# Kernel tuning notes

Measured on AMD Instinct MI355X. Metric: run time of the kernel, lower is better.

## Reference

```python
import jax, jax.numpy as jnp
import numpy as np

B, T, IN, H, OUT = 256, 512, 9, 512, 3


def setup_inputs() -> dict:
    key = jax.random.key(0)
    ks = jax.random.split(key, 7)
    s = 0.05  # keep gates in a sane range
    return {
        "x": jax.random.normal(ks[0], (B, T, IN), dtype=jnp.float32),
        "W_ih": jax.random.normal(ks[1], (4 * H, IN), dtype=jnp.float32) * s,
        "W_hh": jax.random.normal(ks[2], (4 * H, H), dtype=jnp.float32) * s,
        "b_ih": jax.random.normal(ks[3], (4 * H,), dtype=jnp.float32) * s,
        "b_hh": jax.random.normal(ks[4], (4 * H,), dtype=jnp.float32) * s,
        "W_fc": jax.random.normal(ks[5], (OUT, H), dtype=jnp.float32) * s,
        "b_fc": jax.random.normal(ks[6], (OUT,), dtype=jnp.float32) * s,
        "horizon": 10,
    }


def reference(x, W_ih, W_hh, b_ih, b_hh, W_fc, b_fc, horizon):
    Bn, Tn, _ = x.shape
    Hn = W_hh.shape[1]
    On = W_fc.shape[0]
    # branch condition depends only on the static step index -> precompute mask
    idx = np.arange(Tn)
    use_raw = jnp.asarray((idx < 5) | (idx % int(horizon) == 0))  # [T]

    def step(carry, inp):
        hx, cx, prev_out = carry
        x_t, raw = inp  # x_t: [B, IN], raw: scalar bool
        # else-branch input: previous fc output (3) ++ last 6 state features -> 9
        alt = jnp.concatenate([prev_out, x_t[:, On:]], axis=1)
        xin = jnp.where(raw, x_t, alt)
        gates = xin @ W_ih.T + b_ih + hx @ W_hh.T + b_hh  # [B, 4H]
        i, f, g, o = jnp.split(gates, 4, axis=1)
        cx2 = jax.nn.sigmoid(f) * cx + jax.nn.sigmoid(i) * jnp.tanh(g)
        hx2 = jax.nn.sigmoid(o) * jnp.tanh(cx2)
        out = hx2 @ W_fc.T + b_fc  # [B, OUT]
        return (hx2, cx2, out), out

    init = (
        jnp.zeros((Bn, Hn), x.dtype),
        jnp.zeros((Bn, Hn), x.dtype),
        jnp.zeros((Bn, On), x.dtype),
    )
    x_tb = jnp.swapaxes(x, 0, 1)  # [T, B, IN]
    _, outs = jax.lax.scan(step, init, (x_tb, use_raw))
    return jnp.swapaxes(outs, 0, 1)  # [B, T, OUT]
```

## Files before the change

kernel.cpp:

```cpp
#include <hip/hip_runtime.h>

typedef __attribute__((ext_vector_type(8))) short bf16x8;
typedef __attribute__((ext_vector_type(4))) float f32x4;

#define NTT 512
#define NH  512
#define NIN 9
#define NO  3
#define MEMBERS 32
#define MROWS   32
#define HPW     16

__device__ __forceinline__ short f2bf(float f) {
  unsigned u = __builtin_bit_cast(unsigned, f);
  u = (u + 0x7fffu + ((u >> 16) & 1u)) >> 16;
  return (short)u;
}
__device__ __forceinline__ float bf2f(short s) {
  unsigned u = ((unsigned)(unsigned short)s) << 16;
  return __builtin_bit_cast(float, u);
}
__device__ __forceinline__ float sigf(float x) { return 1.f / (1.f + __expf(-x)); }
__device__ __forceinline__ float tanh_fast(float x) { return 1.f - 2.f / (1.f + __expf(2.f * x)); }

__global__ __launch_bounds__(256, 1) void lstm_tagged(
    const float* __restrict__ x, const float* __restrict__ W_ih,
    const float* __restrict__ W_hh, const float* __restrict__ b_ih,
    const float* __restrict__ b_hh, const float* __restrict__ W_fc,
    const float* __restrict__ b_fc, const int* __restrict__ horizon,
    float* __restrict__ out, unsigned* __restrict__ ws32) {
  const int tid  = threadIdx.x;
  const int bid  = blockIdx.x;
  const int g    = bid >> 5;
  const int w    = bid & 31;
  const int wid  = tid >> 6;
  const int lane = tid & 63;
  const int l15  = lane & 15;
  const int quad = lane >> 4;
  const int hl   = tid & 15;
  const int b0   = tid >> 4;
  const int hg   = w * HPW + hl;

  unsigned* tbuf0 = ws32;
  unsigned* tbuf1 = ws32 + 131072;

  __shared__ __align__(16) unsigned short hbuf[32][520];
  __shared__ __align__(16) float gbuf[4][16][36];
  __shared__ float fcbuf[4][32][4];
  __shared__ float xbuf[32][NIN];
  __shared__ float xw[64][NIN];
  __shared__ float bsl[64];

  bf16x8 Bhi[16], Blo[16];
#pragma unroll
  for (int kt = 0; kt < 16; ++kt) {
    bf16x8 vh, vl;
    const int row = wid * NH + w * HPW + l15;
#pragma unroll
    for (int j = 0; j < 8; ++j) {
      int k = kt * 32 + quad * 8 + j;
      float v = W_hh[(size_t)row * NH + k];
      short hi = f2bf(v);
      vh[j] = hi; vl[j] = f2bf(v - bf2f(hi));
    }
    Bhi[kt] = vh; Blo[kt] = vl;
  }
  bf16x8 Fhi[4], Flo[4];
#pragma unroll
  for (int kk = 0; kk < 4; ++kk) {
    bf16x8 vh, vl;
#pragma unroll
    for (int j = 0; j < 8; ++j) {
      int k = (wid * 4 + kk) * 32 + quad * 8 + j;
      float v = (l15 < NO) ? W_fc[(size_t)l15 * NH + k] : 0.f;
      short hi = f2bf(v);
      vh[j] = hi; vl[j] = f2bf(v - bf2f(hi));
    }
    Fhi[kk] = vh; Flo[kk] = vl;
  }
  if (tid < 64) {
    int grow = (tid >> 4) * NH + w * HPW + (tid & 15);
    bsl[tid] = b_ih[grow] + b_hh[grow];
#pragma unroll
    for (int k = 0; k < NIN; ++k) xw[tid][k] = W_ih[grow * NIN + k];
  }
  for (int i = tid; i < 8320; i += 256) ((unsigned*)hbuf)[i] = 0u;
  const float bfc0 = b_fc[0], bfc1 = b_fc[1], bfc2 = b_fc[2];
  const int hor = *horizon;
  __syncthreads();

  float cst[2] = {0.f, 0.f};
  int tmod = 0;

  for (int t = 0; t <= NTT; ++t) {
    float xv0 = 0.f, xv1 = 0.f;
    int r0 = 0, k0 = 0, r1 = 0, k1 = 0;
    if (t < NTT) {
      r0 = tid / NIN; k0 = tid - r0 * NIN;
      if (r0 < MROWS) xv0 = x[((size_t)(g * MROWS + r0) * NTT + t) * NIN + k0];
      int i1 = tid + 256;
      r1 = i1 / NIN; k1 = i1 - r1 * NIN;
      if (i1 < MROWS * NIN) xv1 = x[((size_t)(g * MROWS + r1) * NTT + t) * NIN + k1];
    }

    f32x4 z4 = {0.f, 0.f, 0.f, 0.f};
    f32x4 accg[2] = {z4, z4}, accf[2] = {z4, z4};
#pragma unroll
    for (int kt = 0; kt < 16; ++kt) {
      bf16x8 a0 = *(const bf16x8*)&hbuf[l15][kt * 32 + quad * 8];
      bf16x8 a1 = *(const bf16x8*)&hbuf[16 + l15][kt * 32 + quad * 8];
      accg[0] = __builtin_amdgcn_mfma_f32_16x16x32_bf16(a0, Bhi[kt], accg[0], 0, 0, 0);
      accg[1] = __builtin_amdgcn_mfma_f32_16x16x32_bf16(a1, Bhi[kt], accg[1], 0, 0, 0);
      accg[0] = __builtin_amdgcn_mfma_f32_16x16x32_bf16(a0, Blo[kt], accg[0], 0, 0, 0);
      accg[1] = __builtin_amdgcn_mfma_f32_16x16x32_bf16(a1, Blo[kt], accg[1], 0, 0, 0);
      if ((kt >> 2) == wid) {
        int kk = kt & 3;
        accf[0] = __builtin_amdgcn_mfma_f32_16x16x32_bf16(a0, Fhi[kk], accf[0], 0, 0, 0);
        accf[1] = __builtin_amdgcn_mfma_f32_16x16x32_bf16(a1, Fhi[kk], accf[1], 0, 0, 0);
        accf[0] = __builtin_amdgcn_mfma_f32_16x16x32_bf16(a0, Flo[kk], accf[0], 0, 0, 0);
        accf[1] = __builtin_amdgcn_mfma_f32_16x16x32_bf16(a1, Flo[kk], accf[1], 0, 0, 0);
      }
    }
#pragma unroll
    for (int mt = 0; mt < 2; ++mt)
      *(f32x4*)&gbuf[wid][l15][mt * 16 + quad * 4] = accg[mt];
    if (l15 < NO) {
#pragma unroll
      for (int mt = 0; mt < 2; ++mt)
#pragma unroll
        for (int r = 0; r < 4; ++r) fcbuf[wid][mt * 16 + quad * 4 + r][l15] = accf[mt][r];
    }
    if (t < NTT) {
      if (r0 < MROWS) xbuf[r0][k0] = xv0;
      if (tid < MROWS * NIN - 256) xbuf[r1][k1] = xv1;
    }
    __syncthreads();

    if (t == NTT) {
      if (w == 0 && tid < MROWS * NO) {
        int b = tid / NO, o = tid - b * NO;
        float bo = (o == 0) ? bfc0 : (o == 1) ? bfc1 : bfc2;
        out[((size_t)(g * MROWS + b) * NTT + (t - 1)) * NO + o] =
            bo + fcbuf[0][b][o] + fcbuf[1][b][o] + fcbuf[2][b][o] + fcbuf[3][b][o];
      }
      break;
    }

    const bool raw = (t < 5) || (tmod == 0);
    const unsigned tg = (unsigned)(t + 1);
    unsigned* dst = ((t & 1) ? tbuf1 : tbuf0) + (size_t)g * 16384;

#pragma unroll
    for (int e = 0; e < 2; ++e) {
      int b = b0 + 16 * e;
      float xin[NIN];
#pragma unroll
      for (int k = 0; k < NIN; ++k) xin[k] = xbuf[b][k];
      if (!raw) {
        xin[0] = bfc0 + fcbuf[0][b][0] + fcbuf[1][b][0] + fcbuf[2][b][0] + fcbuf[3][b][0];
        xin[1] = bfc1 + fcbuf[0][b][1] + fcbuf[1][b][1] + fcbuf[2][b][1] + fcbuf[3][b][1];
        xin[2] = bfc2 + fcbuf[0][b][2] + fcbuf[1][b][2] + fcbuf[2][b][2] + fcbuf[3][b][2];
      }
      float gv[4];
#pragma unroll
      for (int gg = 0; gg < 4; ++gg) {
        int r = gg * 16 + hl;
        float s = bsl[r] + gbuf[gg][hl][b];
#pragma unroll
        for (int k = 0; k < NIN; ++k) s += xin[k] * xw[r][k];
        gv[gg] = s;
      }
      float cn = sigf(gv[1]) * cst[e] + sigf(gv[0]) * tanh_fast(gv[2]);
      cst[e] = cn;
      float hn = sigf(gv[3]) * tanh_fast(cn);
      unsigned word = (unsigned)(unsigned short)f2bf(hn) | (tg << 16);
      __hip_atomic_store(&dst[(size_t)b * NH + hg], word,
                         __ATOMIC_RELAXED, __HIP_MEMORY_SCOPE_AGENT);
    }

    if (w == 0 && t > 0 && tid < MROWS * NO) {
      int b = tid / NO, o = tid - b * NO;
      float bo = (o == 0) ? bfc0 : (o == 1) ? bfc1 : bfc2;
      out[((size_t)(g * MROWS + b) * NTT + (t - 1)) * NO + o] =
          bo + fcbuf[0][b][o] + fcbuf[1][b][o] + fcbuf[2][b][o] + fcbuf[3][b][o];
    }

    {
      const unsigned long long* src =
          (const unsigned long long*)(((t & 1) ? tbuf1 : tbuf0) + (size_t)g * 16384);
      const unsigned long long pat =
          ((unsigned long long)tg << 16) | ((unsigned long long)tg << 48);
      unsigned* hb32 = (unsigned*)hbuf;
      for (;;) {
        unsigned long long bad = 0;
#pragma unroll
        for (int bb = 0; bb < 4; ++bb) {
          unsigned long long v[8];
#pragma unroll
          for (int j = 0; j < 8; ++j)
            v[j] = __hip_atomic_load(src + tid + 256 * (bb * 8 + j),
                                     __ATOMIC_RELAXED, __HIP_MEMORY_SCOPE_AGENT);
#pragma unroll
          for (int j = 0; j < 8; ++j) {
            int q = tid + 256 * (bb * 8 + j);
            bad |= (v[j] ^ pat) & 0xFFFF0000FFFF0000ULL;
            unsigned pk = (unsigned)(v[j] & 0xFFFFu) |
                          ((unsigned)(v[j] >> 32) << 16);
            hb32[(q >> 8) * 260 + (q & 255)] = pk;
          }
        }
        if (__syncthreads_count(bad != 0) == 0) break;
        __builtin_amdgcn_s_sleep(1);
      }
    }
    ++tmod; if (tmod == hor) tmod = 0;
  }
}

__global__ __launch_bounds__(256, 1) void lstm_fallback(
    const float* __restrict__ x, const float* __restrict__ W_ih,
    const float* __restrict__ W_hh, const float* __restrict__ b_ih,
    const float* __restrict__ b_hh, const float* __restrict__ W_fc,
    const float* __restrict__ b_fc, const int* __restrict__ horizon,
    float* __restrict__ out, unsigned short* __restrict__ ws) {
  const int tid  = threadIdx.x;
  const int bid  = blockIdx.x;
  const int g    = bid >> 5;
  const int w    = bid & 31;
  const int wid  = tid >> 6;
  const int lane = tid & 63;
  const int l15  = lane & 15;
  const int quad = lane >> 4;
  const int hl   = tid & 15;
  const int b0   = tid >> 4;

  unsigned short* buf0 = ws;
  unsigned short* buf1 = ws + 131072;
  int* fl = (int*)(ws + 262144) + g * MEMBERS;

  __shared__ __align__(16) unsigned short hbuf[32][520];
  __shared__ __align__(16) float gbuf[4][16][36];
  __shared__ float fcbuf[4][32][4];
  __shared__ float xbuf[32][NIN];
  __shared__ float xw[64][NIN];
  __shared__ float bsl[64];

  bf16x8 Bhi[16], Blo[16];
#pragma unroll
  for (int kt = 0; kt < 16; ++kt) {
    bf16x8 vh, vl;
    const int row = wid * NH + w * HPW + l15;
#pragma unroll
    for (int j = 0; j < 8; ++j) {
      int k = kt * 32 + quad * 8 + j;
      float v = W_hh[(size_t)row * NH + k];
      short hi = f2bf(v);
      vh[j] = hi; vl[j] = f2bf(v - bf2f(hi));
    }
    Bhi[kt] = vh; Blo[kt] = vl;
  }
  bf16x8 Fhi[4], Flo[4];
#pragma unroll
  for (int kk = 0; kk < 4; ++kk) {
    bf16x8 vh, vl;
#pragma unroll
    for (int j = 0; j < 8; ++j) {
      int k = (wid * 4 + kk) * 32 + quad * 8 + j;
      float v = (l15 < NO) ? W_fc[(size_t)l15 * NH + k] : 0.f;
      short hi = f2bf(v);
      vh[j] = hi; vl[j] = f2bf(v - bf2f(hi));
    }
    Fhi[kk] = vh; Flo[kk] = vl;
  }
  if (tid < 64) {
    int grow = (tid >> 4) * NH + w * HPW + (tid & 15);
    bsl[tid] = b_ih[grow] + b_hh[grow];
#pragma unroll
    for (int k = 0; k < NIN; ++k) xw[tid][k] = W_ih[grow * NIN + k];
  }
  for (int i = tid; i < 8320; i += 256) ((unsigned*)hbuf)[i] = 0u;
  const float bfc0 = b_fc[0], bfc1 = b_fc[1], bfc2 = b_fc[2];
  const int hor = *horizon;
  __syncthreads();

  float cst[2] = {0.f, 0.f};
  int tmod = 0;

  for (int t = 0; t <= NTT; ++t) {
    float xv0 = 0.f, xv1 = 0.f;
    int r0 = 0, k0 = 0, r1 = 0, k1 = 0;
    if (t < NTT) {
      r0 = tid / NIN; k0 = tid - r0 * NIN;
      if (r0 < MROWS) xv0 = x[((size_t)(g * MROWS + r0) * NTT + t) * NIN + k0];
      int i1 = tid + 256;
      r1 = i1 / NIN; k1 = i1 - r1 * NIN;
      if (i1 < MROWS * NIN) xv1 = x[((size_t)(g * MROWS + r1) * NTT + t) * NIN + k1];
    }
    f32x4 z4 = {0.f, 0.f, 0.f, 0.f};
    f32x4 accg[2] = {z4, z4}, accf[2] = {z4, z4};
#pragma unroll
    for (int kt = 0; kt < 16; ++kt) {
      bf16x8 a0 = *(const bf16x8*)&hbuf[l15][kt * 32 + quad * 8];
      bf16x8 a1 = *(const bf16x8*)&hbuf[16 + l15][kt * 32 + quad * 8];
      accg[0] = __builtin_amdgcn_mfma_f32_16x16x32_bf16(a0, Bhi[kt], accg[0], 0, 0, 0);
      accg[1] = __builtin_amdgcn_mfma_f32_16x16x32_bf16(a1, Bhi[kt], accg[1], 0, 0, 0);
      accg[0] = __builtin_amdgcn_mfma_f32_16x16x32_bf16(a0, Blo[kt], accg[0], 0, 0, 0);
      accg[1] = __builtin_amdgcn_mfma_f32_16x16x32_bf16(a1, Blo[kt], accg[1], 0, 0, 0);
      if ((kt >> 2) == wid) {
        int kk = kt & 3;
        accf[0] = __builtin_amdgcn_mfma_f32_16x16x32_bf16(a0, Fhi[kk], accf[0], 0, 0, 0);
        accf[1] = __builtin_amdgcn_mfma_f32_16x16x32_bf16(a1, Fhi[kk], accf[1], 0, 0, 0);
        accf[0] = __builtin_amdgcn_mfma_f32_16x16x32_bf16(a0, Flo[kk], accf[0], 0, 0, 0);
        accf[1] = __builtin_amdgcn_mfma_f32_16x16x32_bf16(a1, Flo[kk], accf[1], 0, 0, 0);
      }
    }
#pragma unroll
    for (int mt = 0; mt < 2; ++mt)
      *(f32x4*)&gbuf[wid][l15][mt * 16 + quad * 4] = accg[mt];
    if (l15 < NO) {
#pragma unroll
      for (int mt = 0; mt < 2; ++mt)
#pragma unroll
        for (int r = 0; r < 4; ++r) fcbuf[wid][mt * 16 + quad * 4 + r][l15] = accf[mt][r];
    }
    if (t < NTT) {
      if (r0 < MROWS) xbuf[r0][k0] = xv0;
      if (tid < MROWS * NIN - 256) xbuf[r1][k1] = xv1;
    }
    __syncthreads();

    if (t == NTT) {
      if (w == 0 && tid < MROWS * NO) {
        int b = tid / NO, o = tid - b * NO;
        float bo = (o == 0) ? bfc0 : (o == 1) ? bfc1 : bfc2;
        out[((size_t)(g * MROWS + b) * NTT + (t - 1)) * NO + o] =
            bo + fcbuf[0][b][o] + fcbuf[1][b][o] + fcbuf[2][b][o] + fcbuf[3][b][o];
      }
      break;
    }

    const bool raw = (t < 5) || (tmod == 0);
    unsigned long long* nxt64 =
        (unsigned long long*)(((t & 1) ? buf1 : buf0) + (size_t)g * (MROWS * NH));
#pragma unroll
    for (int e = 0; e < 2; ++e) {
      int b = b0 + 16 * e;
      float xin[NIN];
#pragma unroll
      for (int k = 0; k < NIN; ++k) xin[k] = xbuf[b][k];
      if (!raw) {
        xin[0] = bfc0 + fcbuf[0][b][0] + fcbuf[1][b][0] + fcbuf[2][b][0] + fcbuf[3][b][0];
        xin[1] = bfc1 + fcbuf[0][b][1] + fcbuf[1][b][1] + fcbuf[2][b][1] + fcbuf[3][b][1];
        xin[2] = bfc2 + fcbuf[0][b][2] + fcbuf[1][b][2] + fcbuf[2][b][2] + fcbuf[3][b][2];
      }
      float gv[4];
#pragma unroll
      for (int gg = 0; gg < 4; ++gg) {
        int r = gg * 16 + hl;
        float s = bsl[r] + gbuf[gg][hl][b];
#pragma unroll
        for (int k = 0; k < NIN; ++k) s += xin[k] * xw[r][k];
        gv[gg] = s;
      }
      float cn = sigf(gv[1]) * cst[e] + sigf(gv[0]) * tanh_fast(gv[2]);
      cst[e] = cn;
      float hn = sigf(gv[3]) * tanh_fast(cn);
      unsigned hb16 = (unsigned)(unsigned short)f2bf(hn);
      unsigned pair = hb16 | ((unsigned)__shfl_xor((int)hb16, 1, 64) << 16);
      unsigned long long v64 =
          (unsigned long long)pair |
          ((unsigned long long)(unsigned)__shfl_xor((int)pair, 2, 64) << 32);
      if ((hl & 3) == 0)
        __hip_atomic_store(&nxt64[(size_t)b * 128 + w * 4 + (hl >> 2)], v64,
                           __ATOMIC_RELAXED, __HIP_MEMORY_SCOPE_AGENT);
    }
    asm volatile("s_waitcnt vmcnt(0)" ::: "memory");
    __syncthreads();

    if (tid == 0)
      __hip_atomic_store(&fl[w], t + 1, __ATOMIC_RELAXED, __HIP_MEMORY_SCOPE_AGENT);
    if (w == 0 && t > 0 && tid < MROWS * NO) {
      int b = tid / NO, o = tid - b * NO;
      float bo = (o == 0) ? bfc0 : (o == 1) ? bfc1 : bfc2;
      out[((size_t)(g * MROWS + b) * NTT + (t - 1)) * NO + o] =
          bo + fcbuf[0][b][o] + fcbuf[1][b][o] + fcbuf[2][b][o] + fcbuf[3][b][o];
    }
    if (tid < MEMBERS) {
      while (__hip_atomic_load(&fl[tid], __ATOMIC_RELAXED,
                               __HIP_MEMORY_SCOPE_AGENT) < t + 1)
        __builtin_amdgcn_s_sleep(1);
    }
    __syncthreads();

    const unsigned long long* src =
        (const unsigned long long*)(((t & 1) ? buf1 : buf0) + (size_t)g * (MROWS * NH));
#pragma unroll
    for (int j = 0; j < 16; ++j) {
      int idx = tid + 256 * j;
      unsigned long long v =
          __hip_atomic_load(src + idx, __ATOMIC_RELAXED, __HIP_MEMORY_SCOPE_AGENT);
      *(unsigned long long*)&hbuf[idx >> 7][(idx & 127) * 4] = v;
    }
    __syncthreads();
    ++tmod; if (tmod == hor) tmod = 0;
  }
}

extern "C" void kernel_launch(void* const* d_in, const int* in_sizes, int n_in,
                              void* d_out, int out_size, void* d_ws, size_t ws_size,
                              hipStream_t stream) {
  (void)in_sizes; (void)n_in; (void)out_size;
  const float* x    = (const float*)d_in[0];
  const float* W_ih = (const float*)d_in[1];
  const float* W_hh = (const float*)d_in[2];
  const float* b_ih = (const float*)d_in[3];
  const float* b_hh = (const float*)d_in[4];
  const float* W_fc = (const float*)d_in[5];
  const float* b_fc = (const float*)d_in[6];
  const int*   hor  = (const int*)d_in[7];
  if (ws_size >= (size_t)1048576) {
    lstm_tagged<<<dim3(256), dim3(256), 0, stream>>>(
        x, W_ih, W_hh, b_ih, b_hh, W_fc, b_fc, hor,
        (float*)d_out, (unsigned*)d_ws);
  } else {
    lstm_fallback<<<dim3(256), dim3(256), 0, stream>>>(
        x, W_ih, W_hh, b_ih, b_hh, W_fc, b_fc, hor,
        (float*)d_out, (unsigned short*)d_ws);
  }
}
```

Before: 3.201 ms.

## Replace block-wide retry loop with per-word spin waits in hidden-state exchange

The cross-block hidden-state gather used to reload all 32 words per thread and retry as a whole whenever any word in the block was stale, with a block-wide count reduction and a sleep between rounds. It now issues 16 loads at a time and spins on each stale word individually, followed by a single barrier, so already-valid words are never re-read. Loop-invariant index math for the x loads and output stores is also hoisted out of the time loop. The per-word spinning may increase polling traffic on the L2 while a few words lag.

```diff
diff --git a/kernel.cpp b/kernel.cpp
--- a/kernel.cpp
+++ b/kernel.cpp
@@ -87,6 +87,17 @@
   for (int i = tid; i < 8320; i += 256) ((unsigned*)hbuf)[i] = 0u;
   const float bfc0 = b_fc[0], bfc1 = b_fc[1], bfc2 = b_fc[2];
   const int hor = *horizon;
+
+  const int r0c = tid / NIN, k0c = tid - r0c * NIN;
+  const int i1c = tid + 256;
+  const int r1c = i1c / NIN, k1c = i1c - r1c * NIN;
+  const bool x0ok = (r0c < MROWS), x1ok = (i1c < MROWS * NIN);
+  const float* xp0 = x + (size_t)(g * MROWS + (x0ok ? r0c : 0)) * NTT * NIN + k0c;
+  const float* xp1 = x + (size_t)(g * MROWS + (x1ok ? r1c : 0)) * NTT * NIN + k1c;
+  const int ob = tid / NO, oo = tid - ob * NO;
+  const bool ook = (w == 0) && (tid < MROWS * NO);
+  const float obias = (oo == 0) ? bfc0 : (oo == 1) ? bfc1 : bfc2;
+  float* op = out + ((size_t)(g * MROWS + ob) * NTT) * NO + oo;
   __syncthreads();
 
   float cst[2] = {0.f, 0.f};
@@ -94,13 +105,9 @@
 
   for (int t = 0; t <= NTT; ++t) {
     float xv0 = 0.f, xv1 = 0.f;
-    int r0 = 0, k0 = 0, r1 = 0, k1 = 0;
     if (t < NTT) {
-      r0 = tid / NIN; k0 = tid - r0 * NIN;
-      if (r0 < MROWS) xv0 = x[((size_t)(g * MROWS + r0) * NTT + t) * NIN + k0];
-      int i1 = tid + 256;
-      r1 = i1 / NIN; k1 = i1 - r1 * NIN;
-      if (i1 < MROWS * NIN) xv1 = x[((size_t)(g * MROWS + r1) * NTT + t) * NIN + k1];
+      if (x0ok) xv0 = xp0[t * NIN];
+      if (x1ok) xv1 = xp1[t * NIN];
     }
 
     f32x4 z4 = {0.f, 0.f, 0.f, 0.f};
@@ -131,18 +138,15 @@
         for (int r = 0; r < 4; ++r) fcbuf[wid][mt * 16 + quad * 4 + r][l15] = accf[mt][r];
     }
     if (t < NTT) {
-      if (r0 < MROWS) xbuf[r0][k0] = xv0;
-      if (tid < MROWS * NIN - 256) xbuf[r1][k1] = xv1;
+      if (x0ok) xbuf[r0c][k0c] = xv0;
+      if (x1ok) xbuf[r1c][k1c] = xv1;
     }
     __syncthreads();
 
     if (t == NTT) {
-      if (w == 0 && tid < MROWS * NO) {
-        int b = tid / NO, o = tid - b * NO;
-        float bo = (o == 0) ? bfc0 : (o == 1) ? bfc1 : bfc2;
-        out[((size_t)(g * MROWS + b) * NTT + (t - 1)) * NO + o] =
-            bo + fcbuf[0][b][o] + fcbuf[1][b][o] + fcbuf[2][b][o] + fcbuf[3][b][o];
-      }
+      if (ook)
+        op[(t - 1) * NO] =
+            obias + fcbuf[0][ob][oo] + fcbuf[1][ob][oo] + fcbuf[2][ob][oo] + fcbuf[3][ob][oo];
       break;
     }
 
@@ -178,12 +182,9 @@
                          __ATOMIC_RELAXED, __HIP_MEMORY_SCOPE_AGENT);
     }
 
-    if (w == 0 && t > 0 && tid < MROWS * NO) {
-      int b = tid / NO, o = tid - b * NO;
-      float bo = (o == 0) ? bfc0 : (o == 1) ? bfc1 : bfc2;
-      out[((size_t)(g * MROWS + b) * NTT + (t - 1)) * NO + o] =
-          bo + fcbuf[0][b][o] + fcbuf[1][b][o] + fcbuf[2][b][o] + fcbuf[3][b][o];
-    }
+    if (ook && t > 0)
+      op[(t - 1) * NO] =
+          obias + fcbuf[0][ob][oo] + fcbuf[1][ob][oo] + fcbuf[2][ob][oo] + fcbuf[3][ob][oo];
 
     {
       const unsigned long long* src =
@@ -191,27 +192,24 @@
       const unsigned long long pat =
           ((unsigned long long)tg << 16) | ((unsigned long long)tg << 48);
       unsigned* hb32 = (unsigned*)hbuf;
-      for (;;) {
-        unsigned long long bad = 0;
-#pragma unroll
-        for (int bb = 0; bb < 4; ++bb) {
-          unsigned long long v[8];
-#pragma unroll
-          for (int j = 0; j < 8; ++j)
-            v[j] = __hip_atomic_load(src + tid + 256 * (bb * 8 + j),
-                                     __ATOMIC_RELAXED, __HIP_MEMORY_SCOPE_AGENT);
-#pragma unroll
-          for (int j = 0; j < 8; ++j) {
-            int q = tid + 256 * (bb * 8 + j);
-            bad |= (v[j] ^ pat) & 0xFFFF0000FFFF0000ULL;
-            unsigned pk = (unsigned)(v[j] & 0xFFFFu) |
-                          ((unsigned)(v[j] >> 32) << 16);
-            hb32[(q >> 8) * 260 + (q & 255)] = pk;
-          }
+#pragma unroll
+      for (int half = 0; half < 2; ++half) {
+        unsigned long long v[16];
+#pragma unroll
+        for (int j = 0; j < 16; ++j)
+          v[j] = __hip_atomic_load(src + tid + 256 * (half * 16 + j),
+                                   __ATOMIC_RELAXED, __HIP_MEMORY_SCOPE_AGENT);
+#pragma unroll
+        for (int j = 0; j < 16; ++j) {
+          const int q = tid + 256 * (half * 16 + j);
+          while ((v[j] ^ pat) & 0xFFFF0000FFFF0000ULL)
+            v[j] = __hip_atomic_load(src + q, __ATOMIC_RELAXED,
+                                     __HIP_MEMORY_SCOPE_AGENT);
+          hb32[(q >> 8) * 260 + (q & 255)] =
+              (unsigned)(v[j] & 0xFFFFu) | ((unsigned)(v[j] >> 32) << 16);
         }
-        if (__syncthreads_count(bad != 0) == 0) break;
-        __builtin_amdgcn_s_sleep(1);
-      }
+      }
+      __syncthreads();
     }
     ++tmod; if (tmod == hor) tmod = 0;
   }
```

Result: slower. 4.343 ms (+35.7%).
